# Kernel tuning notes

Measured on AMD Instinct MI355X. Metric: run time of the kernel, lower is better.

Reference implementation:

```python
import jax, jax.numpy as jnp
import numpy as np

DIM = 1024
N_HEADS = 16
N_KV_HEADS = 4
HEAD_DIM = DIM // N_HEADS  # 64
N_EXPERTS = 8
TOP_K = 2
ROPE_BASE = 10000.0


def setup_inputs() -> dict:
    key = jax.random.key(0)
    ks = jax.random.split(key, 12)
    B, L, D = 2, 1024, DIM
    s = lambda *sh: 0.02
    inp = {
        "x": jax.random.normal(ks[0], (B, L, D), jnp.float32),
        # attention projections (stored [in, out])
        "wq": jax.random.normal(ks[1], (D, D), jnp.float32) * 0.02,
        "wk": jax.random.normal(ks[2], (D, N_KV_HEADS * HEAD_DIM), jnp.float32) * 0.02,
        "wv": jax.random.normal(ks[3], (D, N_KV_HEADS * HEAD_DIM), jnp.float32) * 0.02,
        "wo": jax.random.normal(ks[4], (D, D), jnp.float32) * 0.02,
        # MoE router + stacked expert FFN weights
        "wg": jax.random.normal(ks[5], (D, N_EXPERTS), jnp.float32) * 0.02,
        "w1": jax.random.normal(ks[6], (N_EXPERTS, D, 4 * D), jnp.float32) * 0.02,
        "w2": jax.random.normal(ks[7], (N_EXPERTS, 4 * D, D), jnp.float32) * 0.02,
        # pre-attention / pre-MoE LayerNorms
        "ln1_g": jnp.ones((D,), jnp.float32),
        "ln1_b": jnp.zeros((D,), jnp.float32),
        "ln2_g": jnp.ones((D,), jnp.float32),
        "ln2_b": jnp.zeros((D,), jnp.float32),
    }
    return inp


def _layernorm(x, g, b, eps=1e-5):
    mu = x.mean(-1, keepdims=True)
    var = ((x - mu) ** 2).mean(-1, keepdims=True)
    return (x - mu) * jax.lax.rsqrt(var + eps) * g + b


def _rope_cos_sin(L, dtype):
    inv_freq = 1.0 / (ROPE_BASE ** (jnp.arange(0, HEAD_DIM, 2, dtype=jnp.float32) / HEAD_DIM))
    t = jnp.arange(L, dtype=jnp.float32)
    freqs = jnp.einsum('i,j->ij', t, inv_freq)          # [L, hd/2]
    emb = jnp.concatenate([freqs, freqs], axis=-1)       # [L, hd]
    return jnp.cos(emb).astype(dtype), jnp.sin(emb).astype(dtype)


def _rotate_half(x):
    x1, x2 = jnp.split(x, 2, axis=-1)
    return jnp.concatenate([-x2, x1], axis=-1)


def _attention(h, wq, wk, wv, wo):
    B, L, D = h.shape
    q = (h @ wq).reshape(B, L, N_HEADS, HEAD_DIM).transpose(0, 2, 1, 3)      # [B,H,L,hd]
    k = (h @ wk).reshape(B, L, N_KV_HEADS, HEAD_DIM).transpose(0, 2, 1, 3)   # [B,Hkv,L,hd]
    v = (h @ wv).reshape(B, L, N_KV_HEADS, HEAD_DIM).transpose(0, 2, 1, 3)
    cos, sin = _rope_cos_sin(L, h.dtype)                  # [L,hd] each
    cos = cos[None, None]; sin = sin[None, None]
    q = q * cos + _rotate_half(q) * sin
    k = k * cos + _rotate_half(k) * sin
    n_rep = N_HEADS // N_KV_HEADS
    k = jnp.repeat(k, n_rep, axis=1)                      # repeat_interleave over head dim
    v = jnp.repeat(v, n_rep, axis=1)
    scores = jnp.einsum('bhqd,bhkd->bhqk', q, k) / jnp.sqrt(jnp.asarray(HEAD_DIM, h.dtype))
    causal = jnp.tril(jnp.ones((L, L), bool))
    scores = jnp.where(causal[None, None], scores, jnp.finfo(scores.dtype).min)
    attn = jax.nn.softmax(scores, axis=-1)
    out = jnp.einsum('bhqk,bhkd->bhqd', attn, v).transpose(0, 2, 1, 3).reshape(B, L, D)
    return out @ wo


def _moe(h, wg, w1, w2):
    B, L, D = h.shape
    gate_logits = h @ wg                                  # [B,L,E]
    top_v, top_i = jax.lax.top_k(gate_logits, TOP_K)      # [B,L,K]
    gates = jax.nn.softmax(top_v, axis=-1)                # [B,L,K]
    one_hot = jax.nn.one_hot(top_i, N_EXPERTS, dtype=h.dtype)   # [B,L,K,E]
    comb = jnp.einsum('blke,blk->ble', one_hot, gates)    # per-token per-expert weight
    # naive MoE: every expert processes every token (as in the source loop)
    hid = jax.nn.gelu(jnp.einsum('bld,edf->eblf', h, w1), approximate=False)  # [E,B,L,4D]
    eout = jnp.einsum('eblf,efd->ebld', hid, w2)          # [E,B,L,D]
    out = jnp.einsum('ebld,ble->bld', eout, comb)
    # load-balance loss from expert assignment counts (buffer starts at zero)
    counts = one_hot.sum(axis=(0, 1, 2))                  # [E]
    counts_norm = counts / counts.sum()
    lb_loss = jnp.mean((counts_norm - 1.0 / N_EXPERTS) ** 2)
    return out, lb_loss


def reference(x, wq, wk, wv, wo, wg, w1, w2, ln1_g, ln1_b, ln2_g, ln2_b):
    h = _layernorm(x, ln1_g, ln1_b)
    x = x + _attention(h, wq, wk, wv, wo)
    h = _layernorm(x, ln2_g, ln2_b)
    moe_out, lb_loss = _moe(h, wg, w1, w2)
    x = x + moe_out
    return x, lb_loss
```

## Files before the change

kernel.cpp:

```cpp
#include <hip/hip_runtime.h>
#include <hip/hip_bf16.h>

#define NTOK   2048
#define DMODEL 1024
#define NEXP   8
#define DFF    4096
#define MAXROWS 5120
#define MAXTILES 40

typedef __attribute__((ext_vector_type(8))) short short8;
typedef __attribute__((ext_vector_type(4))) float float4v;

__device__ __forceinline__ unsigned short f2bf(float f) {
  union { float f; unsigned u; } v; v.f = f;
  unsigned r = v.u + 0x7fffu + ((v.u >> 16) & 1u);
  return (unsigned short)(r >> 16);
}
__device__ __forceinline__ float bf2f(unsigned short h) {
  union { unsigned u; float f; } v; v.u = ((unsigned)h) << 16; return v.f;
}
__device__ __forceinline__ void gl_lds16(const void* g, void* l) {
  __builtin_amdgcn_global_load_lds((const __attribute__((address_space(1))) void*)g,
                                   (__attribute__((address_space(3))) void*)l, 16, 0, 0);
}

template<int EPI, int EMAP>
__launch_bounds__(256, 4)
__global__ void gemm_bt(const unsigned short* __restrict__ A,
                        const unsigned short* __restrict__ B0,
                        float* __restrict__ C,
                        unsigned short* __restrict__ Cbf,
                        const int N, const int K,
                        const int* __restrict__ tmap, const long estride) {
  const int mtile = blockIdx.y;
  const unsigned short* B = B0;
  if (EMAP) {
    int e = tmap[mtile];
    if (e < 0) return;
    B += (size_t)e * (size_t)estride;
  }
  const int n0 = blockIdx.x * 128;
  const int m0 = mtile * 128;
  __shared__ unsigned short sA[128 * 64];
  __shared__ unsigned short sB[128 * 64];
  const int tid  = threadIdx.x;
  const int w    = tid >> 6;
  const int lane = tid & 63;
  const int quad = lane >> 4;
  const int r16  = lane & 15;
  const int wr   = w >> 1;
  const int wc   = w & 1;
  const int rl   = lane >> 3;
  const int csl  = lane & 7;
  const int cg   = csl ^ rl;
  float4v acc[4][4];
#pragma unroll
  for (int i = 0; i < 4; ++i)
#pragma unroll
    for (int j = 0; j < 4; ++j) acc[i][j] = float4v{0.f, 0.f, 0.f, 0.f};

  const unsigned short* Ab = A + (size_t)m0 * K + cg * 8;
  const unsigned short* Bb = B + (size_t)n0 * K + cg * 8;

  for (int k0 = 0; k0 < K; k0 += 64) {
    __syncthreads();
#pragma unroll
    for (int i = 0; i < 4; ++i) {
      const int j = w * 4 + i;
      gl_lds16(Ab + (size_t)(j * 8 + rl) * K + k0, (char*)sA + j * 1024);
      gl_lds16(Bb + (size_t)(j * 8 + rl) * K + k0, (char*)sB + j * 1024);
    }
    __syncthreads();
#pragma unroll
    for (int kc = 0; kc < 8; kc += 4) {
      short8 af[4], bq[4];
#pragma unroll
      for (int mt = 0; mt < 4; ++mt) {
        int r = wr * 64 + mt * 16 + r16;
        af[mt] = *(const short8*)(sA + ((r * 8 + ((kc + quad) ^ (r & 7))) * 8));
      }
#pragma unroll
      for (int nt = 0; nt < 4; ++nt) {
        int r = wc * 64 + nt * 16 + r16;
        bq[nt] = *(const short8*)(sB + ((r * 8 + ((kc + quad) ^ (r & 7))) * 8));
      }
#pragma unroll
      for (int mt = 0; mt < 4; ++mt)
#pragma unroll
        for (int nt = 0; nt < 4; ++nt)
          acc[mt][nt] = __builtin_amdgcn_mfma_f32_16x16x32_bf16(af[mt], bq[nt], acc[mt][nt], 0, 0, 0);
    }
  }
#pragma unroll
  for (int mt = 0; mt < 4; ++mt) {
#pragma unroll
    for (int nt = 0; nt < 4; ++nt) {
#pragma unroll
      for (int rg = 0; rg < 4; ++rg) {
        const int m = m0 + wr * 64 + mt * 16 + quad * 4 + rg;
        const int n = n0 + wc * 64 + nt * 16 + r16;
        const size_t idx = (size_t)m * N + n;
        const float v = acc[mt][nt][rg];
        if (EPI == 0) C[idx] = v;
        else {
          float ge = 0.5f * v * (1.0f + erff(v * 0.70710678118654752440f));
          Cbf[idx] = f2bf(ge);
        }
      }
    }
  }
}

template<int EPI>
__launch_bounds__(256, 2)
__global__ void gemm_split(const unsigned short* __restrict__ Ah,
                           const unsigned short* __restrict__ Al,
                           const unsigned short* __restrict__ Bh,
                           const unsigned short* __restrict__ Bl,
                           float* __restrict__ C, const float* __restrict__ R,
                           const int N, const int K) {
  const int n0 = blockIdx.x * 128;
  const int m0 = blockIdx.y * 128;
  __shared__ unsigned short sAh[128 * 64];
  __shared__ unsigned short sAl[128 * 64];
  __shared__ unsigned short sBh[128 * 64];
  __shared__ unsigned short sBl[128 * 64];
  const int tid  = threadIdx.x;
  const int w    = tid >> 6;
  const int lane = tid & 63;
  const int quad = lane >> 4;
  const int r16  = lane & 15;
  const int wr   = w >> 1;
  const int wc   = w & 1;
  const int rl   = lane >> 3;
  const int csl  = lane & 7;
  const int cg   = csl ^ rl;
  float4v acc[4][4];
#pragma unroll
  for (int i = 0; i < 4; ++i)
#pragma unroll
    for (int j = 0; j < 4; ++j) acc[i][j] = float4v{0.f, 0.f, 0.f, 0.f};

  const size_t aoff = (size_t)m0 * K + cg * 8;
  const size_t boff = (size_t)n0 * K + cg * 8;

  for (int k0 = 0; k0 < K; k0 += 64) {
    __syncthreads();
#pragma unroll
    for (int i = 0; i < 4; ++i) {
      const int j = w * 4 + i;
      const size_t ro = (size_t)(j * 8 + rl) * K + k0;
      gl_lds16(Ah + aoff + ro, (char*)sAh + j * 1024);
      gl_lds16(Al + aoff + ro, (char*)sAl + j * 1024);
      gl_lds16(Bh + boff + ro, (char*)sBh + j * 1024);
      gl_lds16(Bl + boff + ro, (char*)sBl + j * 1024);
    }
    __syncthreads();
#pragma unroll
    for (int kc = 0; kc < 8; kc += 4) {
      short8 afh[4], afl[4], bqh[4], bql[4];
#pragma unroll
      for (int mt = 0; mt < 4; ++mt) {
        int r = wr * 64 + mt * 16 + r16;
        int o = (r * 8 + ((kc + quad) ^ (r & 7))) * 8;
        afh[mt] = *(const short8*)(sAh + o);
        afl[mt] = *(const short8*)(sAl + o);
      }
#pragma unroll
      for (int nt = 0; nt < 4; ++nt) {
        int r = wc * 64 + nt * 16 + r16;
        int o = (r * 8 + ((kc + quad) ^ (r & 7))) * 8;
        bqh[nt] = *(const short8*)(sBh + o);
        bql[nt] = *(const short8*)(sBl + o);
      }
#pragma unroll
      for (int mt = 0; mt < 4; ++mt)
#pragma unroll
        for (int nt = 0; nt < 4; ++nt) {
          acc[mt][nt] = __builtin_amdgcn_mfma_f32_16x16x32_bf16(afh[mt], bqh[nt], acc[mt][nt], 0, 0, 0);
          acc[mt][nt] = __builtin_amdgcn_mfma_f32_16x16x32_bf16(afh[mt], bql[nt], acc[mt][nt], 0, 0, 0);
          acc[mt][nt] = __builtin_amdgcn_mfma_f32_16x16x32_bf16(afl[mt], bqh[nt], acc[mt][nt], 0, 0, 0);
        }
    }
  }
#pragma unroll
  for (int mt = 0; mt < 4; ++mt) {
#pragma unroll
    for (int nt = 0; nt < 4; ++nt) {
#pragma unroll
      for (int rg = 0; rg < 4; ++rg) {
        const int m = m0 + wr * 64 + mt * 16 + quad * 4 + rg;
        const int n = n0 + wc * 64 + nt * 16 + r16;
        const size_t idx = (size_t)m * N + n;
        const float v = acc[mt][nt][rg];
        if (EPI == 0) C[idx] = v;
        else C[idx] = v + R[idx];
      }
    }
  }
}

template<int WLO>
__global__ void transpose_w(const float* __restrict__ in, unsigned short* __restrict__ oh,
                            unsigned short* __restrict__ ol, const int K, const int N,
                            const long istride, const long ostride) {
  const int bz = blockIdx.z;
  in += (size_t)bz * istride;
  oh += (size_t)bz * ostride;
  if (WLO) ol += (size_t)bz * ostride;
  __shared__ float t[64][65];
  const int n0 = blockIdx.x * 64;
  const int k0 = blockIdx.y * 64;
  const int tid = threadIdx.x;
  const int rr = tid >> 4;
  const int c4 = (tid & 15) * 4;
#pragma unroll
  for (int p = 0; p < 4; ++p) {
    const int row = p * 16 + rr;
    const float4 v = *(const float4*)(in + (size_t)(k0 + row) * N + n0 + c4);
    t[row][c4] = v.x; t[row][c4 + 1] = v.y; t[row][c4 + 2] = v.z; t[row][c4 + 3] = v.w;
  }
  __syncthreads();
#pragma unroll
  for (int p = 0; p < 4; ++p) {
    const int n = p * 16 + rr;
    float vs[4];
#pragma unroll
    for (int i = 0; i < 4; ++i) vs[i] = t[c4 + i][n];
    ushort4 h;
    h.x = f2bf(vs[0]); h.y = f2bf(vs[1]); h.z = f2bf(vs[2]); h.w = f2bf(vs[3]);
    const size_t o = (size_t)(n0 + n) * K + k0 + c4;
    *(ushort4*)(oh + o) = h;
    if (WLO) {
      ushort4 lo4;
      lo4.x = f2bf(vs[0] - bf2f(h.x));
      lo4.y = f2bf(vs[1] - bf2f(h.y));
      lo4.z = f2bf(vs[2] - bf2f(h.z));
      lo4.w = f2bf(vs[3] - bf2f(h.w));
      *(ushort4*)(ol + o) = lo4;
    }
  }
}

__global__ void ln_kernel(const float* __restrict__ x, const float* __restrict__ g,
                          const float* __restrict__ b, unsigned short* __restrict__ hi,
                          unsigned short* __restrict__ lo, float* __restrict__ f32o) {
  const int row = blockIdx.x;
  const int tid = threadIdx.x;
  const int w = tid >> 6, lane = tid & 63;
  const float4 v = *(const float4*)(x + (size_t)row * DMODEL + tid * 4);
  float s = v.x + v.y + v.z + v.w;
  float q = v.x * v.x + v.y * v.y + v.z * v.z + v.w * v.w;
#pragma unroll
  for (int o = 32; o; o >>= 1) { s += __shfl_xor(s, o); q += __shfl_xor(q, o); }
  __shared__ float red[8];
  if (lane == 0) { red[w] = s; red[4 + w] = q; }
  __syncthreads();
  s = red[0] + red[1] + red[2] + red[3];
  q = red[4] + red[5] + red[6] + red[7];
  const float mean = s * (1.0f / DMODEL);
  const float var = q * (1.0f / DMODEL) - mean * mean;
  const float rs = rsqrtf(var + 1e-5f);
  const float4 gg = *(const float4*)(g + tid * 4);
  const float4 bb = *(const float4*)(b + tid * 4);
  float y[4];
  y[0] = (v.x - mean) * rs * gg.x + bb.x;
  y[1] = (v.y - mean) * rs * gg.y + bb.y;
  y[2] = (v.z - mean) * rs * gg.z + bb.z;
  y[3] = (v.w - mean) * rs * gg.w + bb.w;
  const size_t base = (size_t)row * DMODEL + tid * 4;
#pragma unroll
  for (int i = 0; i < 4; ++i) {
    unsigned short h = f2bf(y[i]);
    hi[base + i] = h;
    if (lo) lo[base + i] = f2bf(y[i] - bf2f(h));
    if (f32o) f32o[base + i] = y[i];
  }
}

__global__ void rope_split(const float* __restrict__ qkv,
                           unsigned short* __restrict__ q_hi, unsigned short* __restrict__ q_lo,
                           unsigned short* __restrict__ k_hi, unsigned short* __restrict__ k_lo) {
  const int rowtok = blockIdx.x;
  const int b = rowtok >> 10;
  const int l = rowtok & 1023;
  const int tid = threadIdx.x;
  __shared__ float cb[32], sb[32];
  if (tid < 32) {
    float inv = powf(10000.0f, -(float)tid * (1.0f / 32.0f));
    float ang = (float)l * inv;
    cb[tid] = cosf(ang);
    sb[tid] = sinf(ang);
  }
  __syncthreads();
  const float* src = qkv + (size_t)rowtok * 1536;
#pragma unroll
  for (int it = 0; it < 5; ++it) {
    const int e = tid + it * 256;
    const int hh = e >> 6;
    const int d = e & 63;
    const int dm = d & 31;
    float val = src[e];
    float partner = (d < 32) ? -src[e + 32] : src[e - 32];
    float ov = val * cb[dm] + partner * sb[dm];
    unsigned short hv = f2bf(ov);
    unsigned short lv = f2bf(ov - bf2f(hv));
    if (hh < 16) {
      size_t idx = ((size_t)(b * 16 + hh) * 1024 + l) * 64 + d;
      q_hi[idx] = hv; q_lo[idx] = lv;
    } else {
      size_t idx = ((size_t)(b * 4 + (hh - 16)) * 1024 + l) * 64 + d;
      k_hi[idx] = hv; k_lo[idx] = lv;
    }
  }
}

__global__ void vt_split(const float* __restrict__ qkv,
                         unsigned short* __restrict__ vt_hi, unsigned short* __restrict__ vt_lo) {
  const int bkvh = blockIdx.z;
  const int b = bkvh >> 2;
  const int kvh = bkvh & 3;
  const float* src = qkv + (size_t)b * 1024 * 1536 + 1280 + kvh * 64;
  __shared__ float t[32][33];
  const int l0 = blockIdx.y * 32;
  const int d0 = blockIdx.x * 32;
  const int tx = threadIdx.x;
  const int ty = threadIdx.y;
#pragma unroll
  for (int i = 0; i < 4; ++i)
    t[ty + i * 8][tx] = src[(size_t)(l0 + ty + i * 8) * 1536 + d0 + tx];
  __syncthreads();
#pragma unroll
  for (int i = 0; i < 4; ++i) {
    float v = t[tx][ty + i * 8];
    size_t o = (size_t)bkvh * 65536 + (size_t)(d0 + ty + i * 8) * 1024 + l0 + tx;
    unsigned short h = f2bf(v);
    vt_hi[o] = h;
    vt_lo[o] = f2bf(v - bf2f(h));
  }
}

__launch_bounds__(256, 2)
__global__ void attn_mfma(const unsigned short* __restrict__ q_hi, const unsigned short* __restrict__ q_lo,
                          const unsigned short* __restrict__ k_hi, const unsigned short* __restrict__ k_lo,
                          const unsigned short* __restrict__ vt_hi, const unsigned short* __restrict__ vt_lo,
                          unsigned short* __restrict__ ohi, unsigned short* __restrict__ olo) {
  const int blk = blockIdx.x;
  const int bh = blk & 31;
  const int qt = 15 - (blk >> 5);
  const int b = bh >> 4;
  const int h = bh & 15;
  const int kvbh = b * 4 + (h >> 2);
  const int q0 = qt * 64;
  const int tid = threadIdx.x;
  const int w = tid >> 6;
  const int lane = tid & 63;
  const int quad = lane >> 4;
  const int r16 = lane & 15;
  const int rl = lane >> 3;
  const int csl = lane & 7;
  const int cg = csl ^ rl;

  __shared__ unsigned short sK[2][64 * 64];
  __shared__ unsigned short sV[2][64 * 64];
  __shared__ unsigned short sP[2][64 * 64];

  short8 qfh[2], qfl[2];
  {
    const size_t qrow = ((size_t)bh * 1024 + q0 + w * 16 + r16) * 64 + quad * 8;
    qfh[0] = *(const short8*)(q_hi + qrow);
    qfh[1] = *(const short8*)(q_hi + qrow + 32);
    qfl[0] = *(const short8*)(q_lo + qrow);
    qfl[1] = *(const short8*)(q_lo + qrow + 32);
  }
  float4v O[4];
#pragma unroll
  for (int nt = 0; nt < 4; ++nt) O[nt] = float4v{0.f, 0.f, 0.f, 0.f};
  float m[4], l[4];
#pragma unroll
  for (int rg = 0; rg < 4; ++rg) { m[rg] = -__builtin_inff(); l[rg] = 0.f; }

  const unsigned short* khb = k_hi + (size_t)kvbh * 65536 + cg * 8;
  const unsigned short* klb = k_lo + (size_t)kvbh * 65536 + cg * 8;
  const unsigned short* vhb = vt_hi + (size_t)kvbh * 65536 + cg * 8;
  const unsigned short* vlb = vt_lo + (size_t)kvbh * 65536 + cg * 8;

  for (int c = 0; c <= qt; ++c) {
    __syncthreads();
#pragma unroll
    for (int j = 0; j < 2; ++j) {
      const int i = w * 2 + j;
      const int row = i * 8 + rl;
      gl_lds16(khb + (size_t)(c * 64 + row) * 64, (char*)sK[0] + i * 1024);
      gl_lds16(klb + (size_t)(c * 64 + row) * 64, (char*)sK[1] + i * 1024);
      gl_lds16(vhb + (size_t)row * 1024 + c * 64, (char*)sV[0] + i * 1024);
      gl_lds16(vlb + (size_t)row * 1024 + c * 64, (char*)sV[1] + i * 1024);
    }
    __syncthreads();

    float4v S[4];
#pragma unroll
    for (int nt = 0; nt < 4; ++nt) S[nt] = float4v{0.f, 0.f, 0.f, 0.f};
#pragma unroll
    for (int ks = 0; ks < 2; ++ks) {
#pragma unroll
      for (int nt = 0; nt < 4; ++nt) {
        const int r = nt * 16 + r16;
        const int o = (r * 8 + ((ks * 4 + quad) ^ (r & 7))) * 8;
        const short8 kh = *(const short8*)(sK[0] + o);
        const short8 kl = *(const short8*)(sK[1] + o);
        S[nt] = __builtin_amdgcn_mfma_f32_16x16x32_bf16(qfh[ks], kh, S[nt], 0, 0, 0);
        S[nt] = __builtin_amdgcn_mfma_f32_16x16x32_bf16(qfh[ks], kl, S[nt], 0, 0, 0);
        S[nt] = __builtin_amdgcn_mfma_f32_16x16x32_bf16(qfl[ks], kh, S[nt], 0, 0, 0);
      }
    }
    const float NEGINF = -__builtin_inff();
#pragma unroll
    for (int nt = 0; nt < 4; ++nt)
#pragma unroll
      for (int rg = 0; rg < 4; ++rg) S[nt][rg] *= 0.125f;
    if (c == qt) {
#pragma unroll
      for (int nt = 0; nt < 4; ++nt) {
        const int col = nt * 16 + r16;
#pragma unroll
        for (int rg = 0; rg < 4; ++rg) {
          const int row = w * 16 + quad * 4 + rg;
          if (col > row) S[nt][rg] = NEGINF;
        }
      }
    }
    float alpha[4], lsum[4];
#pragma unroll
    for (int rg = 0; rg < 4; ++rg) {
      float mx = fmaxf(fmaxf(S[0][rg], S[1][rg]), fmaxf(S[2][rg], S[3][rg]));
      mx = fmaxf(mx, __shfl_xor(mx, 1));
      mx = fmaxf(mx, __shfl_xor(mx, 2));
      mx = fmaxf(mx, __shfl_xor(mx, 4));
      mx = fmaxf(mx, __shfl_xor(mx, 8));
      const float mn = fmaxf(m[rg], mx);
      alpha[rg] = __expf(m[rg] - mn);
      m[rg] = mn;
      lsum[rg] = 0.f;
    }
#pragma unroll
    for (int nt = 0; nt < 4; ++nt)
#pragma unroll
      for (int rg = 0; rg < 4; ++rg) {
        const float e = __expf(S[nt][rg] - m[rg]);
        S[nt][rg] = e;
        lsum[rg] += e;
      }
#pragma unroll
    for (int rg = 0; rg < 4; ++rg) {
      float ls = lsum[rg];
      ls += __shfl_xor(ls, 1);
      ls += __shfl_xor(ls, 2);
      ls += __shfl_xor(ls, 4);
      ls += __shfl_xor(ls, 8);
      l[rg] = l[rg] * alpha[rg] + ls;
    }
#pragma unroll
    for (int nt = 0; nt < 4; ++nt) {
      const int key = nt * 16 + r16;
      const int chunk = key >> 3;
#pragma unroll
      for (int rg = 0; rg < 4; ++rg) {
        const int r = w * 16 + quad * 4 + rg;
        const int addr = r * 64 + ((chunk ^ (r & 7)) * 8) + (key & 7);
        const float e = S[nt][rg];
        const unsigned short hv = f2bf(e);
        sP[0][addr] = hv;
        sP[1][addr] = f2bf(e - bf2f(hv));
      }
    }
#pragma unroll
    for (int nt = 0; nt < 4; ++nt)
#pragma unroll
      for (int rg = 0; rg < 4; ++rg) O[nt][rg] *= alpha[rg];
#pragma unroll
    for (int ks = 0; ks < 2; ++ks) {
      const int rA = w * 16 + r16;
      const int oA = (rA * 8 + ((ks * 4 + quad) ^ (rA & 7))) * 8;
      const short8 ph = *(const short8*)(sP[0] + oA);
      const short8 pl = *(const short8*)(sP[1] + oA);
#pragma unroll
      for (int nt = 0; nt < 4; ++nt) {
        const int rv = nt * 16 + r16;
        const int ov = (rv * 8 + ((ks * 4 + quad) ^ (rv & 7))) * 8;
        const short8 vh = *(const short8*)(sV[0] + ov);
        const short8 vl = *(const short8*)(sV[1] + ov);
        O[nt] = __builtin_amdgcn_mfma_f32_16x16x32_bf16(ph, vh, O[nt], 0, 0, 0);
        O[nt] = __builtin_amdgcn_mfma_f32_16x16x32_bf16(ph, vl, O[nt], 0, 0, 0);
        O[nt] = __builtin_amdgcn_mfma_f32_16x16x32_bf16(pl, vh, O[nt], 0, 0, 0);
      }
    }
  }
#pragma unroll
  for (int nt = 0; nt < 4; ++nt) {
    const int col = h * 64 + nt * 16 + r16;
#pragma unroll
    for (int rg = 0; rg < 4; ++rg) {
      const int row = q0 + w * 16 + quad * 4 + rg;
      const float ovv = O[nt][rg] / l[rg];
      const size_t idx = ((size_t)b * 1024 + row) * DMODEL + col;
      const unsigned short hv = f2bf(ovv);
      ohi[idx] = hv;
      olo[idx] = f2bf(ovv - bf2f(hv));
    }
  }
}

#define RED6SUM(X) { X += __shfl_xor(X,32); X += __shfl_xor(X,16); X += __shfl_xor(X,8); X += __shfl_xor(X,4); X += __shfl_xor(X,2); X += __shfl_xor(X,1); }

__global__ void router_kernel(const float* __restrict__ h2f, const float* __restrict__ wg,
                              int* __restrict__ tok_e, float* __restrict__ tok_g,
                              int* __restrict__ counts) {
  const int t = blockIdx.x;
  const int lane = threadIdx.x;
  float acc[8] = {0,0,0,0,0,0,0,0};
  const float* hr = h2f + (size_t)t * DMODEL;
  for (int d = lane; d < DMODEL; d += 64) {
    const float hv = hr[d];
    const float4 w0 = *(const float4*)(wg + d * 8);
    const float4 w1_ = *(const float4*)(wg + d * 8 + 4);
    acc[0] += hv * w0.x; acc[1] += hv * w0.y; acc[2] += hv * w0.z; acc[3] += hv * w0.w;
    acc[4] += hv * w1_.x; acc[5] += hv * w1_.y; acc[6] += hv * w1_.z; acc[7] += hv * w1_.w;
  }
#pragma unroll
  for (int e = 0; e < 8; ++e) { RED6SUM(acc[e]); }
  if (lane == 0) {
    int i0 = 0; float v0 = acc[0];
#pragma unroll
    for (int e = 1; e < 8; ++e) if (acc[e] > v0) { v0 = acc[e]; i0 = e; }
    int i1 = -1; float v1 = -__builtin_inff();
#pragma unroll
    for (int e = 0; e < 8; ++e) if (e != i0 && acc[e] > v1) { v1 = acc[e]; i1 = e; }
    const float ex = __expf(v1 - v0);
    const float den = 1.0f + ex;
    tok_e[t * 2] = i0; tok_e[t * 2 + 1] = i1;
    tok_g[t * 2] = 1.0f / den; tok_g[t * 2 + 1] = ex / den;
    atomicAdd(counts + i0, 1);
    atomicAdd(counts + i1, 1);
  }
}

__global__ void finalize_kernel(const int* __restrict__ counts, int* __restrict__ off_pad,
                                int* __restrict__ tile_map, float* __restrict__ lb_out) {
  if (threadIdx.x == 0 && blockIdx.x == 0) {
    int tile = 0, rowoff = 0;
    for (int e = 0; e < NEXP; ++e) {
      off_pad[e] = rowoff;
      const int c = counts[e];
      const int nt = (c + 127) >> 7;
      for (int i = 0; i < nt; ++i) tile_map[tile++] = e;
      rowoff += nt * 128;
    }
    for (; tile < MAXTILES; ++tile) tile_map[tile] = -1;
    float sacc = 0.f;
    for (int e = 0; e < NEXP; ++e) {
      const float cn = (float)counts[e] * (1.0f / 4096.0f);
      const float d = cn - 0.125f;
      sacc += d * d;
    }
    lb_out[0] = sacc * (1.0f / 8.0f);
  }
}

__global__ void scatter_kernel(const int* __restrict__ tok_e, const int* __restrict__ off_pad,
                               int* __restrict__ fill, int* __restrict__ tok_pos,
                               const unsigned short* __restrict__ h2bf, unsigned short* __restrict__ Xg) {
  const int slot = blockIdx.x;
  const int t = slot >> 1;
  __shared__ int sp;
  if (threadIdx.x == 0) {
    const int e = tok_e[slot];
    const int r = atomicAdd(fill + e, 1);
    const int ppos = off_pad[e] + r;
    tok_pos[slot] = ppos;
    sp = ppos;
  }
  __syncthreads();
  const int pos = sp;
  *(uint2*)(Xg + (size_t)pos * DMODEL + threadIdx.x * 4) =
      *(const uint2*)(h2bf + (size_t)t * DMODEL + threadIdx.x * 4);
}

__global__ void combine_kernel(const float* __restrict__ x1, const float* __restrict__ eout,
                               const int* __restrict__ tok_pos, const float* __restrict__ tok_g,
                               float* __restrict__ out) {
  const int t = blockIdx.x;
  const int tid = threadIdx.x;
  const int p0 = tok_pos[t * 2], p1 = tok_pos[t * 2 + 1];
  const float g0 = tok_g[t * 2], g1 = tok_g[t * 2 + 1];
  const size_t o = (size_t)t * DMODEL + tid * 4;
  const float4 a = *(const float4*)(x1 + o);
  const float4 e0 = *(const float4*)(eout + (size_t)p0 * DMODEL + tid * 4);
  const float4 e1 = *(const float4*)(eout + (size_t)p1 * DMODEL + tid * 4);
  float4 r;
  r.x = a.x + g0 * e0.x + g1 * e1.x;
  r.y = a.y + g0 * e0.y + g1 * e1.y;
  r.z = a.z + g0 * e0.z + g1 * e1.z;
  r.w = a.w + g0 * e0.w + g1 * e1.w;
  *(float4*)(out + o) = r;
}

__global__ void init_kernel(int* counts, int* fill) {
  const int t = threadIdx.x;
  if (t < 8) { counts[t] = 0; fill[t] = 0; }
}

extern "C" void kernel_launch(void* const* d_in, const int* in_sizes, int n_in,
                              void* d_out, int out_size, void* d_ws, size_t ws_size,
                              hipStream_t stream) {
  (void)in_sizes; (void)n_in; (void)out_size; (void)ws_size;
  const float* x    = (const float*)d_in[0];
  const float* wq   = (const float*)d_in[1];
  const float* wk   = (const float*)d_in[2];
  const float* wv   = (const float*)d_in[3];
  const float* wo   = (const float*)d_in[4];
  const float* wg   = (const float*)d_in[5];
  const float* w1   = (const float*)d_in[6];
  const float* w2   = (const float*)d_in[7];
  const float* ln1g = (const float*)d_in[8];
  const float* ln1b = (const float*)d_in[9];
  const float* ln2g = (const float*)d_in[10];
  const float* ln2b = (const float*)d_in[11];
  float* out = (float*)d_out;

  char* p = (char*)d_ws;
  auto take = [&](size_t n) { void* r = (void*)p; p += (n + 255) & ~(size_t)255; return r; };
  unsigned short* h1_hi   = (unsigned short*)take((size_t)NTOK * DMODEL * 2);
  unsigned short* h1_lo   = (unsigned short*)take((size_t)NTOK * DMODEL * 2);
  unsigned short* wqkv_hi = (unsigned short*)take((size_t)1536 * 1024 * 2);
  unsigned short* wqkv_lo = (unsigned short*)take((size_t)1536 * 1024 * 2);
  unsigned short* woT_hi  = (unsigned short*)take((size_t)1024 * 1024 * 2);
  unsigned short* woT_lo  = (unsigned short*)take((size_t)1024 * 1024 * 2);
  unsigned short* w1t     = (unsigned short*)take((size_t)NEXP * DFF * DMODEL * 2);
  unsigned short* w2t     = (unsigned short*)take((size_t)NEXP * DMODEL * DFF * 2);
  float* qkv   = (float*)take((size_t)NTOK * 1536 * 4);
  unsigned short* q_hi  = (unsigned short*)take((size_t)2 * 16 * 1024 * 64 * 2);
  unsigned short* q_lo  = (unsigned short*)take((size_t)2 * 16 * 1024 * 64 * 2);
  unsigned short* k_hi  = (unsigned short*)take((size_t)2 * 4 * 1024 * 64 * 2);
  unsigned short* k_lo  = (unsigned short*)take((size_t)2 * 4 * 1024 * 64 * 2);
  unsigned short* vt_hi = (unsigned short*)take((size_t)2 * 4 * 1024 * 64 * 2);
  unsigned short* vt_lo = (unsigned short*)take((size_t)2 * 4 * 1024 * 64 * 2);
  unsigned short* attn_hi = (unsigned short*)take((size_t)NTOK * DMODEL * 2);
  unsigned short* attn_lo = (unsigned short*)take((size_t)NTOK * DMODEL * 2);
  float* x1    = (float*)take((size_t)NTOK * DMODEL * 4);
  float* h2f   = (float*)take((size_t)NTOK * DMODEL * 4);
  unsigned short* h2bf = (unsigned short*)take((size_t)NTOK * DMODEL * 2);
  unsigned short* Xg   = (unsigned short*)take((size_t)MAXROWS * DMODEL * 2);
  unsigned short* hid  = (unsigned short*)take((size_t)MAXROWS * DFF * 2);
  float* eout  = (float*)take((size_t)MAXROWS * DMODEL * 4);
  int*   tok_e   = (int*)take(4096 * 4);
  float* tok_g   = (float*)take(4096 * 4);
  int*   tok_pos = (int*)take(4096 * 4);
  int*   counts  = (int*)take(64);
  int*   fill    = (int*)take(64);
  int*   off_pad = (int*)take(64);
  int*   tile_map = (int*)take(256);

  init_kernel<<<1, 64, 0, stream>>>(counts, fill);
  ln_kernel<<<NTOK, 256, 0, stream>>>(x, ln1g, ln1b, h1_hi, h1_lo, nullptr);
  transpose_w<1><<<dim3(16, 16, 1), 256, 0, stream>>>(wq, wqkv_hi, wqkv_lo, 1024, 1024, 0, 0);
  transpose_w<1><<<dim3(4, 16, 1), 256, 0, stream>>>(wk, wqkv_hi + (size_t)1024 * 1024, wqkv_lo + (size_t)1024 * 1024, 1024, 256, 0, 0);
  transpose_w<1><<<dim3(4, 16, 1), 256, 0, stream>>>(wv, wqkv_hi + (size_t)1280 * 1024, wqkv_lo + (size_t)1280 * 1024, 1024, 256, 0, 0);
  transpose_w<1><<<dim3(16, 16, 1), 256, 0, stream>>>(wo, woT_hi, woT_lo, 1024, 1024, 0, 0);
  transpose_w<0><<<dim3(64, 16, 8), 256, 0, stream>>>(w1, w1t, nullptr, 1024, 4096, (long)1024 * 4096, (long)4096 * 1024);
  transpose_w<0><<<dim3(16, 64, 8), 256, 0, stream>>>(w2, w2t, nullptr, 4096, 1024, (long)4096 * 1024, (long)1024 * 4096);
  gemm_split<0><<<dim3(12, 16), 256, 0, stream>>>(h1_hi, h1_lo, wqkv_hi, wqkv_lo, qkv, nullptr, 1536, 1024);
  rope_split<<<NTOK, 256, 0, stream>>>(qkv, q_hi, q_lo, k_hi, k_lo);
  vt_split<<<dim3(2, 32, 8), dim3(32, 8), 0, stream>>>(qkv, vt_hi, vt_lo);
  attn_mfma<<<512, 256, 0, stream>>>(q_hi, q_lo, k_hi, k_lo, vt_hi, vt_lo, attn_hi, attn_lo);
  gemm_split<2><<<dim3(8, 16), 256, 0, stream>>>(attn_hi, attn_lo, woT_hi, woT_lo, x1, x, 1024, 1024);
  ln_kernel<<<NTOK, 256, 0, stream>>>(x1, ln2g, ln2b, h2bf, nullptr, h2f);
  router_kernel<<<NTOK, 64, 0, stream>>>(h2f, wg, tok_e, tok_g, counts);
  finalize_kernel<<<1, 64, 0, stream>>>(counts, off_pad, tile_map, out + (size_t)NTOK * DMODEL);
  scatter_kernel<<<4096, 256, 0, stream>>>(tok_e, off_pad, fill, tok_pos, h2bf, Xg);
  gemm_bt<3,1><<<dim3(32, MAXTILES), 256, 0, stream>>>(Xg, w1t, nullptr, hid, DFF, DMODEL, tile_map, (long)DFF * DMODEL);
  gemm_bt<0,1><<<dim3(8, MAXTILES), 256, 0, stream>>>(hid, w2t, eout, nullptr, DMODEL, DFF, tile_map, (long)DMODEL * DFF);
  combine_kernel<<<NTOK, 256, 0, stream>>>(x1, eout, tok_pos, tok_g, out);
}
```

Baseline: 757.2 us.

## Split-K the QKV, output-projection and expert down-projection GEMMs

Adds a blockIdx.z K-slice to gemm_bt and gemm_split so the QKV projection (2 slices), the Wo projection (4 slices) and the w2 expert GEMM (4 slices) each write partial sums into separate buffers. The partial sums are then added in the consumers: rope_split/vt_split, a new merge_x1 kernel that also adds the residual, and combine_kernel. The goal is to raise block count on these small-grid GEMMs so more CUs are busy. In exchange it adds extra fp32 partial-buffer traffic and one more kernel launch.

New measurement: 716.3 us. -5.4%, faster.

```diff
diff --git a/kernel.cpp b/kernel.cpp
--- a/kernel.cpp
+++ b/kernel.cpp
@@ -31,6 +31,7 @@
                         float* __restrict__ C,
                         unsigned short* __restrict__ Cbf,
                         const int N, const int K,
+                        const int kslice, const long zstride,
                         const int* __restrict__ tmap, const long estride) {
   const int mtile = blockIdx.y;
   const unsigned short* B = B0;
@@ -41,6 +42,7 @@
   }
   const int n0 = blockIdx.x * 128;
   const int m0 = mtile * 128;
+  if (EPI == 0) C += (size_t)blockIdx.z * (size_t)zstride;
   __shared__ unsigned short sA[128 * 64];
   __shared__ unsigned short sB[128 * 64];
   const int tid  = threadIdx.x;
@@ -62,7 +64,9 @@
   const unsigned short* Ab = A + (size_t)m0 * K + cg * 8;
   const unsigned short* Bb = B + (size_t)n0 * K + cg * 8;
 
-  for (int k0 = 0; k0 < K; k0 += 64) {
+  const int kbeg = blockIdx.z * kslice;
+  const int kend = kbeg + kslice;
+  for (int k0 = kbeg; k0 < kend; k0 += 64) {
     __syncthreads();
 #pragma unroll
     for (int i = 0; i < 4; ++i) {
@@ -111,16 +115,17 @@
   }
 }
 
-template<int EPI>
 __launch_bounds__(256, 2)
 __global__ void gemm_split(const unsigned short* __restrict__ Ah,
                            const unsigned short* __restrict__ Al,
                            const unsigned short* __restrict__ Bh,
                            const unsigned short* __restrict__ Bl,
-                           float* __restrict__ C, const float* __restrict__ R,
-                           const int N, const int K) {
+                           float* __restrict__ C,
+                           const int N, const int K,
+                           const int kslice, const long zstride) {
   const int n0 = blockIdx.x * 128;
   const int m0 = blockIdx.y * 128;
+  C += (size_t)blockIdx.z * (size_t)zstride;
   __shared__ unsigned short sAh[128 * 64];
   __shared__ unsigned short sAl[128 * 64];
   __shared__ unsigned short sBh[128 * 64];
@@ -144,7 +149,9 @@
   const size_t aoff = (size_t)m0 * K + cg * 8;
   const size_t boff = (size_t)n0 * K + cg * 8;
 
-  for (int k0 = 0; k0 < K; k0 += 64) {
+  const int kbeg = blockIdx.z * kslice;
+  const int kend = kbeg + kslice;
+  for (int k0 = kbeg; k0 < kend; k0 += 64) {
     __syncthreads();
 #pragma unroll
     for (int i = 0; i < 4; ++i) {
@@ -191,10 +198,7 @@
       for (int rg = 0; rg < 4; ++rg) {
         const int m = m0 + wr * 64 + mt * 16 + quad * 4 + rg;
         const int n = n0 + wc * 64 + nt * 16 + r16;
-        const size_t idx = (size_t)m * N + n;
-        const float v = acc[mt][nt][rg];
-        if (EPI == 0) C[idx] = v;
-        else C[idx] = v + R[idx];
+        C[(size_t)m * N + n] = acc[mt][nt][rg];
       }
     }
   }
@@ -278,7 +282,7 @@
   }
 }
 
-__global__ void rope_split(const float* __restrict__ qkv,
+__global__ void rope_split(const float* __restrict__ qkv, const float* __restrict__ qkv2,
                            unsigned short* __restrict__ q_hi, unsigned short* __restrict__ q_lo,
                            unsigned short* __restrict__ k_hi, unsigned short* __restrict__ k_lo) {
   const int rowtok = blockIdx.x;
@@ -293,15 +297,16 @@
     sb[tid] = sinf(ang);
   }
   __syncthreads();
-  const float* src = qkv + (size_t)rowtok * 1536;
+  const float* src  = qkv  + (size_t)rowtok * 1536;
+  const float* src2 = qkv2 + (size_t)rowtok * 1536;
 #pragma unroll
   for (int it = 0; it < 5; ++it) {
     const int e = tid + it * 256;
     const int hh = e >> 6;
     const int d = e & 63;
     const int dm = d & 31;
-    float val = src[e];
-    float partner = (d < 32) ? -src[e + 32] : src[e - 32];
+    float val = src[e] + src2[e];
+    float partner = (d < 32) ? -(src[e + 32] + src2[e + 32]) : (src[e - 32] + src2[e - 32]);
     float ov = val * cb[dm] + partner * sb[dm];
     unsigned short hv = f2bf(ov);
     unsigned short lv = f2bf(ov - bf2f(hv));
@@ -315,20 +320,24 @@
   }
 }
 
-__global__ void vt_split(const float* __restrict__ qkv,
+__global__ void vt_split(const float* __restrict__ qkv, const float* __restrict__ qkv2,
                          unsigned short* __restrict__ vt_hi, unsigned short* __restrict__ vt_lo) {
   const int bkvh = blockIdx.z;
   const int b = bkvh >> 2;
   const int kvh = bkvh & 3;
-  const float* src = qkv + (size_t)b * 1024 * 1536 + 1280 + kvh * 64;
+  const size_t sbase = (size_t)b * 1024 * 1536 + 1280 + kvh * 64;
+  const float* src  = qkv  + sbase;
+  const float* src2 = qkv2 + sbase;
   __shared__ float t[32][33];
   const int l0 = blockIdx.y * 32;
   const int d0 = blockIdx.x * 32;
   const int tx = threadIdx.x;
   const int ty = threadIdx.y;
 #pragma unroll
-  for (int i = 0; i < 4; ++i)
-    t[ty + i * 8][tx] = src[(size_t)(l0 + ty + i * 8) * 1536 + d0 + tx];
+  for (int i = 0; i < 4; ++i) {
+    const size_t o = (size_t)(l0 + ty + i * 8) * 1536 + d0 + tx;
+    t[ty + i * 8][tx] = src[o] + src2[o];
+  }
   __syncthreads();
 #pragma unroll
   for (int i = 0; i < 4; ++i) {
@@ -511,6 +520,18 @@
   }
 }
 
+__global__ void merge_x1(const float* __restrict__ x, const float* __restrict__ parts,
+                         float* __restrict__ x1) {
+  const size_t i = ((size_t)blockIdx.x * 256 + threadIdx.x) * 4;
+  float4 r = *(const float4*)(x + i);
+#pragma unroll
+  for (int z = 0; z < 4; ++z) {
+    const float4 p = *(const float4*)(parts + (size_t)z * NTOK * DMODEL + i);
+    r.x += p.x; r.y += p.y; r.z += p.z; r.w += p.w;
+  }
+  *(float4*)(x1 + i) = r;
+}
+
 #define RED6SUM(X) { X += __shfl_xor(X,32); X += __shfl_xor(X,16); X += __shfl_xor(X,8); X += __shfl_xor(X,4); X += __shfl_xor(X,2); X += __shfl_xor(X,1); }
 
 __global__ void router_kernel(const float* __restrict__ h2f, const float* __restrict__ wg,
@@ -595,13 +616,21 @@
   const float g0 = tok_g[t * 2], g1 = tok_g[t * 2 + 1];
   const size_t o = (size_t)t * DMODEL + tid * 4;
   const float4 a = *(const float4*)(x1 + o);
-  const float4 e0 = *(const float4*)(eout + (size_t)p0 * DMODEL + tid * 4);
-  const float4 e1 = *(const float4*)(eout + (size_t)p1 * DMODEL + tid * 4);
+  float s0x = 0.f, s0y = 0.f, s0z = 0.f, s0w = 0.f;
+  float s1x = 0.f, s1y = 0.f, s1z = 0.f, s1w = 0.f;
+#pragma unroll
+  for (int z = 0; z < 4; ++z) {
+    const size_t zb = (size_t)z * MAXROWS * DMODEL;
+    const float4 e0 = *(const float4*)(eout + zb + (size_t)p0 * DMODEL + tid * 4);
+    const float4 e1 = *(const float4*)(eout + zb + (size_t)p1 * DMODEL + tid * 4);
+    s0x += e0.x; s0y += e0.y; s0z += e0.z; s0w += e0.w;
+    s1x += e1.x; s1y += e1.y; s1z += e1.z; s1w += e1.w;
+  }
   float4 r;
-  r.x = a.x + g0 * e0.x + g1 * e1.x;
-  r.y = a.y + g0 * e0.y + g1 * e1.y;
-  r.z = a.z + g0 * e0.z + g1 * e1.z;
-  r.w = a.w + g0 * e0.w + g1 * e1.w;
+  r.x = a.x + g0 * s0x + g1 * s1x;
+  r.y = a.y + g0 * s0y + g1 * s1y;
+  r.z = a.z + g0 * s0z + g1 * s1z;
+  r.w = a.w + g0 * s0w + g1 * s1w;
   *(float4*)(out + o) = r;
 }
 
@@ -638,7 +667,7 @@
   unsigned short* woT_lo  = (unsigned short*)take((size_t)1024 * 1024 * 2);
   unsigned short* w1t     = (unsigned short*)take((size_t)NEXP * DFF * DMODEL * 2);
   unsigned short* w2t     = (unsigned short*)take((size_t)NEXP * DMODEL * DFF * 2);
-  float* qkv   = (float*)take((size_t)NTOK * 1536 * 4);
+  float* qkv   = (float*)take((size_t)2 * NTOK * 1536 * 4);
   unsigned short* q_hi  = (unsigned short*)take((size_t)2 * 16 * 1024 * 64 * 2);
   unsigned short* q_lo  = (unsigned short*)take((size_t)2 * 16 * 1024 * 64 * 2);
   unsigned short* k_hi  = (unsigned short*)take((size_t)2 * 4 * 1024 * 64 * 2);
@@ -647,12 +676,13 @@
   unsigned short* vt_lo = (unsigned short*)take((size_t)2 * 4 * 1024 * 64 * 2);
   unsigned short* attn_hi = (unsigned short*)take((size_t)NTOK * DMODEL * 2);
   unsigned short* attn_lo = (unsigned short*)take((size_t)NTOK * DMODEL * 2);
+  float* x1p   = (float*)take((size_t)4 * NTOK * DMODEL * 4);
   float* x1    = (float*)take((size_t)NTOK * DMODEL * 4);
   float* h2f   = (float*)take((size_t)NTOK * DMODEL * 4);
   unsigned short* h2bf = (unsigned short*)take((size_t)NTOK * DMODEL * 2);
   unsigned short* Xg   = (unsigned short*)take((size_t)MAXROWS * DMODEL * 2);
   unsigned short* hid  = (unsigned short*)take((size_t)MAXROWS * DFF * 2);
-  float* eout  = (float*)take((size_t)MAXROWS * DMODEL * 4);
+  float* eout  = (float*)take((size_t)4 * MAXROWS * DMODEL * 4);
   int*   tok_e   = (int*)take(4096 * 4);
   float* tok_g   = (float*)take(4096 * 4);
   int*   tok_pos = (int*)take(4096 * 4);
@@ -669,16 +699,17 @@
   transpose_w<1><<<dim3(16, 16, 1), 256, 0, stream>>>(wo, woT_hi, woT_lo, 1024, 1024, 0, 0);
   transpose_w<0><<<dim3(64, 16, 8), 256, 0, stream>>>(w1, w1t, nullptr, 1024, 4096, (long)1024 * 4096, (long)4096 * 1024);
   transpose_w<0><<<dim3(16, 64, 8), 256, 0, stream>>>(w2, w2t, nullptr, 4096, 1024, (long)4096 * 1024, (long)1024 * 4096);
-  gemm_split<0><<<dim3(12, 16), 256, 0, stream>>>(h1_hi, h1_lo, wqkv_hi, wqkv_lo, qkv, nullptr, 1536, 1024);
-  rope_split<<<NTOK, 256, 0, stream>>>(qkv, q_hi, q_lo, k_hi, k_lo);
-  vt_split<<<dim3(2, 32, 8), dim3(32, 8), 0, stream>>>(qkv, vt_hi, vt_lo);
+  gemm_split<<<dim3(12, 16, 2), 256, 0, stream>>>(h1_hi, h1_lo, wqkv_hi, wqkv_lo, qkv, 1536, 1024, 512, (long)NTOK * 1536);
+  rope_split<<<NTOK, 256, 0, stream>>>(qkv, qkv + (size_t)NTOK * 1536, q_hi, q_lo, k_hi, k_lo);
+  vt_split<<<dim3(2, 32, 8), dim3(32, 8), 0, stream>>>(qkv, qkv + (size_t)NTOK * 1536, vt_hi, vt_lo);
   attn_mfma<<<512, 256, 0, stream>>>(q_hi, q_lo, k_hi, k_lo, vt_hi, vt_lo, attn_hi, attn_lo);
-  gemm_split<2><<<dim3(8, 16), 256, 0, stream>>>(attn_hi, attn_lo, woT_hi, woT_lo, x1, x, 1024, 1024);
+  gemm_split<<<dim3(8, 16, 4), 256, 0, stream>>>(attn_hi, attn_lo, woT_hi, woT_lo, x1p, 1024, 1024, 256, (long)NTOK * DMODEL);
+  merge_x1<<<2048, 256, 0, stream>>>(x, x1p, x1);
   ln_kernel<<<NTOK, 256, 0, stream>>>(x1, ln2g, ln2b, h2bf, nullptr, h2f);
   router_kernel<<<NTOK, 64, 0, stream>>>(h2f, wg, tok_e, tok_g, counts);
   finalize_kernel<<<1, 64, 0, stream>>>(counts, off_pad, tile_map, out + (size_t)NTOK * DMODEL);
   scatter_kernel<<<4096, 256, 0, stream>>>(tok_e, off_pad, fill, tok_pos, h2bf, Xg);
-  gemm_bt<3,1><<<dim3(32, MAXTILES), 256, 0, stream>>>(Xg, w1t, nullptr, hid, DFF, DMODEL, tile_map, (long)DFF * DMODEL);
-  gemm_bt<0,1><<<dim3(8, MAXTILES), 256, 0, stream>>>(hid, w2t, eout, nullptr, DMODEL, DFF, tile_map, (long)DMODEL * DFF);
+  gemm_bt<3,1><<<dim3(32, MAXTILES), 256, 0, stream>>>(Xg, w1t, nullptr, hid, DFF, DMODEL, DMODEL, 0, tile_map, (long)DFF * DMODEL);
+  gemm_bt<0,1><<<dim3(8, MAXTILES, 4), 256, 0, stream>>>(hid, w2t, eout, nullptr, DMODEL, DFF, 1024, (long)MAXROWS * DMODEL, tile_map, (long)DMODEL * DFF);
   combine_kernel<<<NTOK, 256, 0, stream>>>(x1, eout, tok_pos, tok_g, out);
 }
```
